# Kernel tuning notes

Hardware: AMD Instinct MI355X
Metric: run time of the kernel (lower is better)

Reference implementation:

```python
import jax, jax.numpy as jnp
import numpy as np

OUT, IN, GS = 16384, 4096, 16
G = OUT * IN // GS  # 4194304 groups


def setup_inputs() -> dict:
    key = jax.random.key(0)
    k1, k2, k3, k4 = jax.random.split(key, 4)
    x = jax.random.normal(k1, (8, 32, IN), dtype=jnp.float32)
    weight_q2 = jax.random.randint(k2, (G, GS // 4), 0, 256, dtype=jnp.int32)
    weight_norm = jax.random.uniform(k3, (G, 1), dtype=jnp.float16)
    bias = jax.random.normal(k4, (OUT,), dtype=jnp.float32)
    return {"x": x, "weight_q2": weight_q2, "weight_norm": weight_norm, "bias": bias}


def _dequant_2bit(weight_q2, weight_norm):
    # torch: xq_out[:, i::4] = (xq >> 2i) & 3  =>  element index within group = i + 4*k
    # where k = packed column (slow, stride 4), i = shift index (fast).
    norm = weight_norm.astype(jnp.float32)                      # [G, 1]
    shifts = jnp.arange(4, dtype=jnp.int32) * 2                 # [4]
    vals = (weight_q2[:, :, None] >> shifts) & 3                # [G, 4(pack k), 4(shift i)]
    xq_out = vals.astype(jnp.float32).reshape(G, GS)            # [G, 16], layout k*4 + i
    w = (xq_out / 3.0) * (2.0 * norm) - norm                    # [G, 16]
    return w.reshape(OUT, IN)


def reference(x, weight_q2, weight_norm, bias):
    w = _dequant_2bit(weight_q2, weight_norm)                   # [OUT, IN] fp32
    return jnp.einsum('bsi,oi->bso', x, w) + bias
```

## Files before the change

kernel.cpp:

```cpp
#include <hip/hip_runtime.h>
#include <stdint.h>

#define M_DIM 256
#define N_DIM 16384
#define K_DIM 4096
#define BM 128
#define BN 64
#define BK 64

typedef __bf16 bf16x8 __attribute__((ext_vector_type(8)));
typedef float  f32x4  __attribute__((ext_vector_type(4)));

__device__ __forceinline__ uint32_t f2bf(float f) {
  uint32_t u = __float_as_uint(f);
  return (u + 0x7fffu + ((u >> 16) & 1u)) >> 16;
}

__global__ __launch_bounds__(256) void cvt_x_kernel(const float* __restrict__ x,
                                                    uint4* __restrict__ ws) {
  int T = blockIdx.x * 256 + threadIdx.x;
  int mb_glob = T >> 13;
  int r       = T & 8191;
  int kch     = r >> 6;
  int L       = r & 63;
  int row = mb_glob * 16 + (L & 15);
  int k   = kch * 32 + (L >> 4) * 8;
  const float* p = x + (size_t)row * K_DIM + k;
  float4 a = *(const float4*)p;
  float4 b = *(const float4*)(p + 4);
  uint4 o;
  o.x = f2bf(a.x) | (f2bf(a.y) << 16);
  o.y = f2bf(a.z) | (f2bf(a.w) << 16);
  o.z = f2bf(b.x) | (f2bf(b.y) << 16);
  o.w = f2bf(b.z) | (f2bf(b.w) << 16);
  ws[T] = o;
}

__global__ __launch_bounds__(256, 2) void gemm2bit_kernel(
    const uint4*    __restrict__ aws,
    const uint32_t* __restrict__ q2,
    const float*    __restrict__ nrm,
    const float*    __restrict__ bias,
    float*          __restrict__ out)
{
  __shared__ uint4 Ab[1024];
  __shared__ uint4 Bb[512];

  const int tid  = threadIdx.x;
  const int lane = tid & 63;
  const int w    = tid >> 6;
  const int wm   = w >> 1;
  const int wn   = w & 1;
  const int lo4  = lane & 15;
  const int qd   = lane >> 4;

  const int n0 = blockIdx.x * BN;
  const int m0 = blockIdx.y * BM;

  const int snb  = tid >> 6;
  const int sqd  = (tid >> 4) & 3;
  const int slo4 = tid & 15;
  const int grow = n0 + snb * 16 + slo4;

  f32x4 acc[4][2];
#pragma unroll
  for (int s = 0; s < 4; ++s)
#pragma unroll
    for (int u = 0; u < 2; ++u)
      acc[s][u] = (f32x4){0.f, 0.f, 0.f, 0.f};

  for (int kc = 0; kc < K_DIM; kc += BK) {
    __syncthreads();

#pragma unroll
    for (int j = 0; j < 4; ++j) {
      int s_lin = j * 256 + tid;
      int ca = s_lin >> 6;
      int L  = s_lin & 63;
      int ts = ca >> 3, mb = ca & 7;
      uint4 g = aws[((size_t)(blockIdx.y * 8 + mb) * 128 + (kc >> 5) + ts) * 64 + L];
      Ab[ca * 64 + L] = g;
    }

    {
      int gidx = grow * 256 + (kc >> 4) + sqd;
      uint4 q  = *(const uint4*)(q2 + (size_t)gidx * 4);
      float nv = nrm[gidx];
      float a  = nv * (2.0f / 3.0f);
      float b  = -nv;
      uint32_t res[8];
#pragma unroll
      for (int p = 0; p < 4; ++p) {
        uint32_t qq = (&q.x)[p];
        float f0 = fmaf((float)(qq & 3u), a, b);
        float f1 = fmaf((float)((qq >> 2) & 3u), a, b);
        float f2 = fmaf((float)((qq >> 4) & 3u), a, b);
        float f3 = fmaf((float)((qq >> 6) & 3u), a, b);
        res[p * 2]     = f2bf(f0) | (f2bf(f1) << 16);
        res[p * 2 + 1] = f2bf(f2) | (f2bf(f3) << 16);
      }
      int cb   = (sqd >> 1) * 4 + snb;
      int base = cb * 64 + (sqd & 1) * 32 + slo4;
      Bb[base]      = make_uint4(res[0], res[1], res[2], res[3]);
      Bb[base + 16] = make_uint4(res[4], res[5], res[6], res[7]);
    }

    __syncthreads();

#pragma unroll
    for (int ts = 0; ts < 2; ++ts) {
      bf16x8 af[4], bf[2];
#pragma unroll
      for (int s = 0; s < 4; ++s)
        af[s] = *(const bf16x8*)&Ab[(ts * 8 + wm * 4 + s) * 64 + lane];
#pragma unroll
      for (int u = 0; u < 2; ++u)
        bf[u] = *(const bf16x8*)&Bb[(ts * 4 + wn * 2 + u) * 64 + lane];
#pragma unroll
      for (int s = 0; s < 4; ++s)
#pragma unroll
        for (int u = 0; u < 2; ++u)
          acc[s][u] = __builtin_amdgcn_mfma_f32_16x16x32_bf16(
              af[s], bf[u], acc[s][u], 0, 0, 0);
    }
  }

  float bv[2];
#pragma unroll
  for (int u = 0; u < 2; ++u)
    bv[u] = bias[n0 + wn * 32 + u * 16 + lo4];

#pragma unroll
  for (int s = 0; s < 4; ++s) {
    int mrow = m0 + wm * 64 + s * 16 + qd * 4;
#pragma unroll
    for (int u = 0; u < 2; ++u) {
      int ncol = n0 + wn * 32 + u * 16 + lo4;
      float* p = out + (size_t)mrow * N_DIM + ncol;
#pragma unroll
      for (int r = 0; r < 4; ++r)
        p[(size_t)r * N_DIM] = acc[s][u][r] + bv[u];
    }
  }
}

extern "C" void kernel_launch(void* const* d_in, const int* in_sizes, int n_in,
                              void* d_out, int out_size, void* d_ws, size_t ws_size,
                              hipStream_t stream) {
  const float*    x    = (const float*)d_in[0];
  const uint32_t* q2   = (const uint32_t*)d_in[1];
  const float*    nm   = (const float*)d_in[2];
  const float*    bias = (const float*)d_in[3];
  float*          out  = (float*)d_out;
  uint4*          aws  = (uint4*)d_ws;

  cvt_x_kernel<<<512, 256, 0, stream>>>(x, aws);

  dim3 grid(N_DIM / BN, M_DIM / BM);
  gemm2bit_kernel<<<grid, 256, 0, stream>>>(aws, q2, nm, bias, out);
}
```

Baseline: 178.6 us.

## Restructure 2-bit GEMM: full-M blocks, split-K warps, register-prefetched A, LUT dequant

Each block now covers all 256 rows with 512 threads, so every weight tile is dequantized once instead of once per M half. Warps split K between two halves and reduce through shared memory at the end. A fragments are loaded straight from global into registers with one-tile-ahead prefetch, which removes the A shared-memory staging. Packed weights are prefetched two tiles ahead into a double-buffered B tile. Dequant now builds the four possible bf16 values once and selects them with byte-permute instead of per-element FMA and conversion. The cost is higher register pressure from 16 accumulators plus prefetch registers, and an extra shared-memory reduction.

After: 166.9 us. 6.6% less time.

```diff
diff --git a/kernel.cpp b/kernel.cpp
--- a/kernel.cpp
+++ b/kernel.cpp
@@ -4,9 +4,9 @@
 #define M_DIM 256
 #define N_DIM 16384
 #define K_DIM 4096
-#define BM 128
 #define BN 64
 #define BK 64
+#define NT (K_DIM / BK)
 
 typedef __bf16 bf16x8 __attribute__((ext_vector_type(8)));
 typedef float  f32x4  __attribute__((ext_vector_type(4)));
@@ -36,111 +36,150 @@
   ws[T] = o;
 }
 
-__global__ __launch_bounds__(256, 2) void gemm2bit_kernel(
+__device__ __forceinline__ uint4 deq8(uint2 q, float nv) {
+  float a2 = nv * (2.0f / 3.0f);
+  uint32_t tlo = f2bf(-nv) | (f2bf(fmaf(1.0f, a2, -nv)) << 16);
+  uint32_t thi = f2bf(fmaf(2.0f, a2, -nv)) | (f2bf(fmaf(3.0f, a2, -nv)) << 16);
+  uint32_t s0 = ((q.x & 3u) | ((q.x & 0xCu) << 14)) * 0x0202u + 0x01000100u;
+  uint32_t s1 = (((q.x >> 4) & 3u) | ((q.x & 0xC0u) << 10)) * 0x0202u + 0x01000100u;
+  uint32_t s2 = ((q.y & 3u) | ((q.y & 0xCu) << 14)) * 0x0202u + 0x01000100u;
+  uint32_t s3 = (((q.y >> 4) & 3u) | ((q.y & 0xC0u) << 10)) * 0x0202u + 0x01000100u;
+  uint4 r;
+  r.x = __builtin_amdgcn_perm(thi, tlo, s0);
+  r.y = __builtin_amdgcn_perm(thi, tlo, s1);
+  r.z = __builtin_amdgcn_perm(thi, tlo, s2);
+  r.w = __builtin_amdgcn_perm(thi, tlo, s3);
+  return r;
+}
+
+__global__ __launch_bounds__(512, 2) void gemm2bit_kernel(
     const uint4*    __restrict__ aws,
     const uint32_t* __restrict__ q2,
     const float*    __restrict__ nrm,
     const float*    __restrict__ bias,
     float*          __restrict__ out)
 {
-  __shared__ uint4 Ab[1024];
-  __shared__ uint4 Bb[512];
+  __shared__ uint4 Bb[2][512];
+  __shared__ uint4 Sc[2048];
 
   const int tid  = threadIdx.x;
   const int lane = tid & 63;
   const int w    = tid >> 6;
   const int wm   = w >> 1;
-  const int wn   = w & 1;
+  const int tw   = w & 1;
   const int lo4  = lane & 15;
   const int qd   = lane >> 4;
+  const int n0   = blockIdx.x * BN;
 
-  const int n0 = blockIdx.x * BN;
-  const int m0 = blockIdx.y * BM;
+  const int nloc = tid >> 3;
+  const int kg   = (tid >> 1) & 3;
+  const int h    = tid & 1;
+  const int grow = n0 + nloc;
+  const int bslot = ((kg >> 1) * 4 + (nloc >> 4)) * 64 + (kg & 1) * 32 + h * 16 + (nloc & 15);
 
-  const int snb  = tid >> 6;
-  const int sqd  = (tid >> 4) & 3;
-  const int slo4 = tid & 15;
-  const int grow = n0 + snb * 16 + slo4;
+  const uint4* pA = aws + (((size_t)(wm * 4) * 128 + tw) * 64 + lane);
+  const uint32_t* pq = q2 + ((size_t)grow * 256 + kg) * 4 + h * 2;
+  const float*    pn = nrm + (size_t)grow * 256 + kg;
 
-  f32x4 acc[4][2];
+  f32x4 acc[4][4];
 #pragma unroll
   for (int s = 0; s < 4; ++s)
 #pragma unroll
-    for (int u = 0; u < 2; ++u)
+    for (int u = 0; u < 4; ++u)
       acc[s][u] = (f32x4){0.f, 0.f, 0.f, 0.f};
 
-  for (int kc = 0; kc < K_DIM; kc += BK) {
-    __syncthreads();
+  uint4 af0[4], af1[4];
+  uint2 qA, qB;
+  float nA, nB;
 
 #pragma unroll
-    for (int j = 0; j < 4; ++j) {
-      int s_lin = j * 256 + tid;
-      int ca = s_lin >> 6;
-      int L  = s_lin & 63;
-      int ts = ca >> 3, mb = ca & 7;
-      uint4 g = aws[((size_t)(blockIdx.y * 8 + mb) * 128 + (kc >> 5) + ts) * 64 + L];
-      Ab[ca * 64 + L] = g;
-    }
+  for (int s = 0; s < 4; ++s) af0[s] = pA[(size_t)s * 8192];
+  uint2 q0 = *(const uint2*)pq;
+  float n0v = pn[0];
+  qA = *(const uint2*)(pq + 16);
+  nA = pn[4];
+  Bb[0][bslot] = deq8(q0, n0v);
+  __syncthreads();
 
-    {
-      int gidx = grow * 256 + (kc >> 4) + sqd;
-      uint4 q  = *(const uint4*)(q2 + (size_t)gidx * 4);
-      float nv = nrm[gidx];
-      float a  = nv * (2.0f / 3.0f);
-      float b  = -nv;
-      uint32_t res[8];
+#define GEMM_BODY(T, PR, AFC, AFN, QC, NC, QN, NN)                              \
+  do {                                                                          \
+    if ((T) + 1 < NT) {                                                         \
+      size_t toff = (size_t)((T) + 1) * 128;                                    \
+      _Pragma("unroll")                                                         \
+      for (int s = 0; s < 4; ++s) AFN[s] = pA[(size_t)s * 8192 + toff];         \
+    }                                                                           \
+    if ((T) + 2 < NT) {                                                         \
+      QN = *(const uint2*)(pq + (size_t)((T) + 2) * 16);                        \
+      NN = pn[(size_t)((T) + 2) * 4];                                           \
+    }                                                                           \
+    bf16x8 bfv[4];                                                              \
+    _Pragma("unroll")                                                           \
+    for (int u = 0; u < 4; ++u)                                                 \
+      bfv[u] = *(const bf16x8*)&Bb[PR][(tw * 4 + u) * 64 + lane];               \
+    _Pragma("unroll")                                                           \
+    for (int s = 0; s < 4; ++s) {                                               \
+      bf16x8 av = __builtin_bit_cast(bf16x8, AFC[s]);                           \
+      _Pragma("unroll")                                                         \
+      for (int u = 0; u < 4; ++u)                                               \
+        acc[s][u] = __builtin_amdgcn_mfma_f32_16x16x32_bf16(av, bfv[u],         \
+                                                            acc[s][u], 0, 0, 0);\
+    }                                                                           \
+    if ((T) + 1 < NT) Bb[(PR) ^ 1][bslot] = deq8(QC, NC);                       \
+    __syncthreads();                                                            \
+  } while (0)
+
+  for (int t2 = 0; t2 < NT; t2 += 2) {
+    GEMM_BODY(t2,     0, af0, af1, qA, nA, qB, nB);
+    GEMM_BODY(t2 + 1, 1, af1, af0, qB, nB, qA, nA);
+  }
+#undef GEMM_BODY
+
+  float bv[4];
 #pragma unroll
-      for (int p = 0; p < 4; ++p) {
-        uint32_t qq = (&q.x)[p];
-        float f0 = fmaf((float)(qq & 3u), a, b);
-        float f1 = fmaf((float)((qq >> 2) & 3u), a, b);
-        float f2 = fmaf((float)((qq >> 4) & 3u), a, b);
-        float f3 = fmaf((float)((qq >> 6) & 3u), a, b);
-        res[p * 2]     = f2bf(f0) | (f2bf(f1) << 16);
-        res[p * 2 + 1] = f2bf(f2) | (f2bf(f3) << 16);
+  for (int u = 0; u < 4; ++u) bv[u] = bias[n0 + u * 16 + lo4];
+
+  if (tw == 1) {
+#pragma unroll
+    for (int s = 0; s < 2; ++s)
+#pragma unroll
+      for (int u = 0; u < 4; ++u)
+        Sc[((wm * 2 + s) * 4 + u) * 64 + lane] = __builtin_bit_cast(uint4, acc[s][u]);
+  }
+  __syncthreads();
+  if (tw == 0) {
+#pragma unroll
+    for (int s = 0; s < 2; ++s)
+#pragma unroll
+      for (int u = 0; u < 4; ++u) {
+        f32x4 o = acc[s][u] +
+                  __builtin_bit_cast(f32x4, Sc[((wm * 2 + s) * 4 + u) * 64 + lane]);
+        int mrow = wm * 64 + s * 16 + qd * 4;
+        float* p = out + (size_t)mrow * N_DIM + (n0 + u * 16 + lo4);
+#pragma unroll
+        for (int r = 0; r < 4; ++r) p[(size_t)r * N_DIM] = o[r] + bv[u];
       }
-      int cb   = (sqd >> 1) * 4 + snb;
-      int base = cb * 64 + (sqd & 1) * 32 + slo4;
-      Bb[base]      = make_uint4(res[0], res[1], res[2], res[3]);
-      Bb[base + 16] = make_uint4(res[4], res[5], res[6], res[7]);
-    }
-
-    __syncthreads();
-
+  }
+  __syncthreads();
+  if (tw == 0) {
 #pragma unroll
-    for (int ts = 0; ts < 2; ++ts) {
-      bf16x8 af[4], bf[2];
+    for (int s = 2; s < 4; ++s)
 #pragma unroll
-      for (int s = 0; s < 4; ++s)
-        af[s] = *(const bf16x8*)&Ab[(ts * 8 + wm * 4 + s) * 64 + lane];
+      for (int u = 0; u < 4; ++u)
+        Sc[((wm * 2 + (s - 2)) * 4 + u) * 64 + lane] = __builtin_bit_cast(uint4, acc[s][u]);
+  }
+  __syncthreads();
+  if (tw == 1) {
 #pragma unroll
-      for (int u = 0; u < 2; ++u)
-        bf[u] = *(const bf16x8*)&Bb[(ts * 4 + wn * 2 + u) * 64 + lane];
+    for (int s = 2; s < 4; ++s)
 #pragma unroll
-      for (int s = 0; s < 4; ++s)
+      for (int u = 0; u < 4; ++u) {
+        f32x4 o = acc[s][u] +
+                  __builtin_bit_cast(f32x4, Sc[((wm * 2 + (s - 2)) * 4 + u) * 64 + lane]);
+        int mrow = wm * 64 + s * 16 + qd * 4;
+        float* p = out + (size_t)mrow * N_DIM + (n0 + u * 16 + lo4);
 #pragma unroll
-        for (int u = 0; u < 2; ++u)
-          acc[s][u] = __builtin_amdgcn_mfma_f32_16x16x32_bf16(
-              af[s], bf[u], acc[s][u], 0, 0, 0);
-    }
-  }
-
-  float bv[2];
-#pragma unroll
-  for (int u = 0; u < 2; ++u)
-    bv[u] = bias[n0 + wn * 32 + u * 16 + lo4];
-
-#pragma unroll
-  for (int s = 0; s < 4; ++s) {
-    int mrow = m0 + wm * 64 + s * 16 + qd * 4;
-#pragma unroll
-    for (int u = 0; u < 2; ++u) {
-      int ncol = n0 + wn * 32 + u * 16 + lo4;
-      float* p = out + (size_t)mrow * N_DIM + ncol;
-#pragma unroll
-      for (int r = 0; r < 4; ++r)
-        p[(size_t)r * N_DIM] = acc[s][u][r] + bv[u];
-    }
+        for (int r = 0; r < 4; ++r) p[(size_t)r * N_DIM] = o[r] + bv[u];
+      }
   }
 }
 
@@ -155,7 +194,5 @@
   uint4*          aws  = (uint4*)d_ws;
 
   cvt_x_kernel<<<512, 256, 0, stream>>>(x, aws);
-
-  dim3 grid(N_DIM / BN, M_DIM / BM);
-  gemm2bit_kernel<<<grid, 256, 0, stream>>>(aws, q2, nm, bias, out);
+  gemm2bit_kernel<<<dim3(N_DIM / BN, 1), 512, 0, stream>>>(aws, q2, nm, bias, out);
 }
```
